# Kernel optimization log

Measured on AMD Instinct MI355X. Metric: run time of the kernel, lower is better.

## Reference

```python
import jax, jax.numpy as jnp
import numpy as np

B, L, D = 2, 4096, 1024
H = 8
DK = D // H          # 128 head qk dim (expand_k=1)
DV = 2 * D // H      # 256 head v dim (expand_v=2)
FFN = 4 * D          # 4096
CHUNK = 64
EPS = 1e-6


def _ln(x, w, b):
    mu = x.mean(-1, keepdims=True)
    var = ((x - mu) ** 2).mean(-1, keepdims=True)
    return (x - mu) / jnp.sqrt(var + EPS) * w + b


def _retention(q, k, v):
    # q,k: [B,H,L,DK], v: [B,H,L,DV]; RetNet decayed causal linear attention,
    # computed chunkwise (intra-chunk parallel + inter-chunk recurrent state).
    Bq, Hq, Lq, Dk = q.shape
    Dv = v.shape[-1]
    N = Lq // CHUNK
    b = 1.0 - jnp.exp2(-5.0 - jnp.arange(Hq, dtype=q.dtype))   # [H] per-head decay
    logb = jnp.log(b)
    q = q * (Dk ** -0.5)
    t = jnp.arange(CHUNK, dtype=q.dtype)
    diff = t[:, None] - t[None, :]                              # [C,C]
    mask = jnp.where(diff >= 0, jnp.exp(logb[:, None, None] * diff), 0.0)  # [H,C,C]
    d_q = jnp.exp(logb[:, None] * (t[None, :] + 1.0))           # b^(t+1), [H,C]
    d_k = jnp.exp(logb[:, None] * (CHUNK - 1.0 - t[None, :]))   # b^(C-1-s), [H,C]
    d_c = jnp.exp(logb * CHUNK)                                 # b^C, [H]

    def to_chunks(x):
        return x.reshape(Bq, Hq, N, CHUNK, -1).transpose(2, 0, 1, 3, 4)  # [N,B,H,C,d]

    qc, kc, vc = to_chunks(q), to_chunks(k), to_chunks(v)
    S0 = jnp.zeros((Bq, Hq, Dk, Dv), q.dtype)

    def step(S, inp):
        qi, ki, vi = inp                                        # [B,H,C,*]
        A = jnp.einsum('bhtd,bhsd->bhts', qi, ki) * mask        # intra-chunk scores
        o = jnp.einsum('bhts,bhsv->bhtv', A, vi)
        o = o + jnp.einsum('bhtd,bhdv->bhtv', qi * d_q[None, :, :, None], S)
        S = S * d_c[None, :, None, None] + jnp.einsum('bhsd,bhsv->bhdv', ki * d_k[None, :, :, None], vi)
        return S, o

    _, os = jax.lax.scan(step, S0, (qc, kc, vc))                # os: [N,B,H,C,DV]
    return os.transpose(1, 2, 0, 3, 4).reshape(Bq, Hq, Lq, Dv)


def setup_inputs() -> dict:
    key = jax.random.key(0)
    ks = jax.random.split(key, 8)
    s = 0.02
    return {
        'x': jax.random.normal(ks[0], (B, L, D), jnp.float32),
        'ln1_w': jnp.ones((D,), jnp.float32),
        'ln1_b': jnp.zeros((D,), jnp.float32),
        'Wq': jax.random.normal(ks[1], (D, D), jnp.float32) * s,
        'Wk': jax.random.normal(ks[2], (D, D), jnp.float32) * s,
        'Wv': jax.random.normal(ks[3], (D, 2 * D), jnp.float32) * s,
        'Wo': jax.random.normal(ks[4], (2 * D, D), jnp.float32) * s,
        'ln2_w': jnp.ones((D,), jnp.float32),
        'ln2_b': jnp.zeros((D,), jnp.float32),
        'W1': jax.random.normal(ks[5], (D, FFN), jnp.float32) * s,
        'b1': jnp.zeros((FFN,), jnp.float32),
        'W2': jax.random.normal(ks[6], (FFN, D), jnp.float32) * s,
        'b2': jnp.zeros((D,), jnp.float32),
    }


def reference(x, ln1_w, ln1_b, Wq, Wk, Wv, Wo, ln2_w, ln2_b, W1, b1, W2, b2):
    # retention branch
    h = _ln(x, ln1_w, ln1_b)
    q = (h @ Wq).reshape(B, L, H, DK).transpose(0, 2, 1, 3)
    k = (h @ Wk).reshape(B, L, H, DK).transpose(0, 2, 1, 3)
    v = (h @ Wv).reshape(B, L, H, DV).transpose(0, 2, 1, 3)
    o = _retention(q, k, v)                                      # [B,H,L,DV]
    o = o.transpose(0, 2, 1, 3).reshape(B, L, H * DV)
    x = x + o @ Wo
    # FFN branch (exact gelu, no subln, eval-mode dropout)
    f = _ln(x, ln2_w, ln2_b)
    f = jax.nn.gelu(f @ W1 + b1, approximate=False)
    x = x + (f @ W2 + b2)
    return x
```

## Files before the change

kernel.cpp:

```cpp
#include <hip/hip_runtime.h>
#include <math.h>

typedef short s16;
typedef __attribute__((ext_vector_type(8))) short short8;
typedef __attribute__((ext_vector_type(4))) float f32x4;

__device__ __forceinline__ float bf2f_lo(unsigned u){ return __builtin_bit_cast(float, u << 16); }
__device__ __forceinline__ float bf2f_hi(unsigned u){ return __builtin_bit_cast(float, u & 0xffff0000u); }
__device__ __forceinline__ float bf2f(unsigned short h){ return __builtin_bit_cast(float, (unsigned)h << 16); }
__device__ __forceinline__ s16 f2bf(float f){
  unsigned u = __builtin_bit_cast(unsigned, f);
  u += 0x7fffu + ((u >> 16) & 1u);
  return (s16)(u >> 16);
}
__device__ __forceinline__ void unpack8(int4 v, float* f){
  unsigned a=(unsigned)v.x, b=(unsigned)v.y, c=(unsigned)v.z, d=(unsigned)v.w;
  f[0]=bf2f_lo(a); f[1]=bf2f_hi(a); f[2]=bf2f_lo(b); f[3]=bf2f_hi(b);
  f[4]=bf2f_lo(c); f[5]=bf2f_hi(c); f[6]=bf2f_lo(d); f[7]=bf2f_hi(d);
}
__device__ __forceinline__ void gl2lds16(const s16* g, s16* l){
  __builtin_amdgcn_global_load_lds((const __attribute__((address_space(1))) void*)g,
                                   (__attribute__((address_space(3))) void*)l, 16, 0, 0);
}

__global__ __launch_bounds__(256) void ln_bf16(const float* __restrict__ x,
                                               const float* __restrict__ w,
                                               const float* __restrict__ b,
                                               s16* __restrict__ out){
  int row = blockIdx.x; int t = threadIdx.x;
  const float* xr = x + (size_t)row * 1024;
  float4 v = *(const float4*)(xr + t*4);
  float s = v.x + v.y + v.z + v.w;
  float ss = v.x*v.x + v.y*v.y + v.z*v.z + v.w*v.w;
  for (int o = 32; o > 0; o >>= 1){ s += __shfl_down(s, o, 64); ss += __shfl_down(ss, o, 64); }
  __shared__ float red[8];
  int wid = t >> 6, lane = t & 63;
  if (lane == 0){ red[wid] = s; red[4+wid] = ss; }
  __syncthreads();
  if (t == 0){
    float S = red[0]+red[1]+red[2]+red[3];
    float SS = red[4]+red[5]+red[6]+red[7];
    red[0] = S * (1.f/1024.f);
    red[1] = SS * (1.f/1024.f);
  }
  __syncthreads();
  float mu = red[0];
  float var = red[1] - mu*mu;
  float rstd = rsqrtf(var + 1e-6f);
  float vv[4] = {v.x, v.y, v.z, v.w};
  short4 o4;
  s16 tmp[4];
  #pragma unroll
  for (int i = 0; i < 4; ++i){
    int c = t*4 + i;
    float val = (vv[i] - mu) * rstd * w[c] + b[c];
    tmp[i] = f2bf(val);
  }
  o4.x = tmp[0]; o4.y = tmp[1]; o4.z = tmp[2]; o4.w = tmp[3];
  *(short4*)(out + (size_t)row*1024 + t*4) = o4;
}

__global__ __launch_bounds__(256) void conv_t(const float* __restrict__ W,
                                              s16* __restrict__ Wt,
                                              int K, int N, float scale){
  __shared__ float tile[32][33];
  int n0 = blockIdx.x * 32, k0 = blockIdx.y * 32;
  int tx = threadIdx.x & 31, ty = threadIdx.x >> 5;
  #pragma unroll
  for (int i = 0; i < 4; ++i){
    int r = ty + i*8;
    tile[r][tx] = W[(size_t)(k0 + r)*N + n0 + tx];
  }
  __syncthreads();
  #pragma unroll
  for (int i = 0; i < 4; ++i){
    int r = ty + i*8;
    Wt[(size_t)(n0 + r)*K + k0 + tx] = f2bf(tile[tx][r] * scale);
  }
}

__device__ __forceinline__ void xcd_tile(int tiles_y, int& tx, int& ty){
  int id = blockIdx.x;
  int sy = tiles_y >> 3;
  int xcd = id & 7, p = id >> 3;
  ty = xcd * sy + (p % sy);
  tx = p / sy;
}

__global__ __launch_bounds__(256,2) void gemm_nt(const s16* __restrict__ A,
                                                 const s16* __restrict__ Bt,
                                                 int M, int N, int K, int ldb,
                                                 float* __restrict__ Cf,
                                                 s16* __restrict__ Cb,
                                                 const float* __restrict__ bias,
                                                 const float* __restrict__ resid,
                                                 int flags, int tiles_y){
  __shared__ s16 As0[128*32], As1[128*32];
  __shared__ s16 Bs0[128*32], Bs1[128*32];
  int t = threadIdx.x;
  int tx, ty; xcd_tile(tiles_y, tx, ty);
  int m0 = ty * 128, n0 = tx * 128;
  int w = t >> 6, lane = t & 63;
  int wm = (w >> 1) * 64, wn = (w & 1) * 64;
  int lrow = lane & 15, lq = lane >> 4;
  f32x4 acc[4][4];
  #pragma unroll
  for (int i = 0; i < 4; ++i)
    #pragma unroll
    for (int j = 0; j < 4; ++j) acc[i][j] = (f32x4){0.f,0.f,0.f,0.f};

  const s16* Ag = A  + (size_t)(m0 + (t>>2)) * K   + (t&3)*8;
  const s16* Bg = Bt + (size_t)(n0 + (t>>2)) * ldb + (t&3)*8;
  int wo = w*512;

  for (int k0 = 0; k0 < K; k0 += 64){
    __syncthreads();
    gl2lds16(Ag + k0,                     As0 + wo);
    gl2lds16(Ag + (size_t)64*K + k0,      As0 + 2048 + wo);
    gl2lds16(Ag + k0 + 32,                As1 + wo);
    gl2lds16(Ag + (size_t)64*K + k0 + 32, As1 + 2048 + wo);
    gl2lds16(Bg + k0,                       Bs0 + wo);
    gl2lds16(Bg + (size_t)64*ldb + k0,      Bs0 + 2048 + wo);
    gl2lds16(Bg + k0 + 32,                  Bs1 + wo);
    gl2lds16(Bg + (size_t)64*ldb + k0 + 32, Bs1 + 2048 + wo);
    __syncthreads();
    short8 af[4], bfr[4];
    #pragma unroll
    for (int mi = 0; mi < 4; ++mi)
      af[mi] = *(short8*)&As0[(wm + mi*16 + lrow)*32 + lq*8];
    #pragma unroll
    for (int ni = 0; ni < 4; ++ni)
      bfr[ni] = *(short8*)&Bs0[(wn + ni*16 + lrow)*32 + lq*8];
    #pragma unroll
    for (int mi = 0; mi < 4; ++mi)
      #pragma unroll
      for (int ni = 0; ni < 4; ++ni)
        acc[mi][ni] = __builtin_amdgcn_mfma_f32_16x16x32_bf16(af[mi], bfr[ni], acc[mi][ni], 0, 0, 0);
    #pragma unroll
    for (int mi = 0; mi < 4; ++mi)
      af[mi] = *(short8*)&As1[(wm + mi*16 + lrow)*32 + lq*8];
    #pragma unroll
    for (int ni = 0; ni < 4; ++ni)
      bfr[ni] = *(short8*)&Bs1[(wn + ni*16 + lrow)*32 + lq*8];
    #pragma unroll
    for (int mi = 0; mi < 4; ++mi)
      #pragma unroll
      for (int ni = 0; ni < 4; ++ni)
        acc[mi][ni] = __builtin_amdgcn_mfma_f32_16x16x32_bf16(af[mi], bfr[ni], acc[mi][ni], 0, 0, 0);
  }

  bool do_gelu = flags & 1;
  bool out_bf = flags & 2;
  #pragma unroll
  for (int mi = 0; mi < 4; ++mi){
    #pragma unroll
    for (int ni = 0; ni < 4; ++ni){
      int gcol = n0 + wn + ni*16 + lrow;
      float bcol = bias ? bias[gcol] : 0.f;
      int grow_base = m0 + wm + mi*16 + lq*4;
      #pragma unroll
      for (int r = 0; r < 4; ++r){
        int grow = grow_base + r;
        float val = acc[mi][ni][r] + bcol;
        if (do_gelu) val = 0.5f * val * (1.f + erff(val * 0.70710678118654752f));
        if (resid) val += resid[(size_t)grow * N + gcol];
        if (out_bf) Cb[(size_t)grow * N + gcol] = f2bf(val);
        else        Cf[(size_t)grow * N + gcol] = val;
      }
    }
  }
}

__global__ __launch_bounds__(256,2) void gemm_nt_h(const s16* __restrict__ A,
                                                   const s16* __restrict__ Bt,
                                                   int M, int N, int K, int ldb,
                                                   float* __restrict__ Cf,
                                                   s16* __restrict__ Cb,
                                                   const float* __restrict__ bias,
                                                   const float* __restrict__ resid,
                                                   int flags, int tiles_y){
  __shared__ s16 As0[64*32], As1[64*32];
  __shared__ s16 Bs0[128*32], Bs1[128*32];
  int t = threadIdx.x;
  int tx, ty; xcd_tile(tiles_y, tx, ty);
  int m0 = ty * 64, n0 = tx * 128;
  int w = t >> 6, lane = t & 63;
  int lrow = lane & 15, lq = lane >> 4;
  f32x4 acc[4][2];
  #pragma unroll
  for (int i = 0; i < 4; ++i)
    #pragma unroll
    for (int j = 0; j < 2; ++j) acc[i][j] = (f32x4){0.f,0.f,0.f,0.f};

  const s16* Ag = A  + (size_t)(m0 + (t>>2)) * K   + (t&3)*8;
  const s16* Bg = Bt + (size_t)(n0 + (t>>2)) * ldb + (t&3)*8;
  int wo = w*512;

  for (int k0 = 0; k0 < K; k0 += 64){
    __syncthreads();
    gl2lds16(Ag + k0,      As0 + wo);
    gl2lds16(Ag + k0 + 32, As1 + wo);
    gl2lds16(Bg + k0,                       Bs0 + wo);
    gl2lds16(Bg + (size_t)64*ldb + k0,      Bs0 + 2048 + wo);
    gl2lds16(Bg + k0 + 32,                  Bs1 + wo);
    gl2lds16(Bg + (size_t)64*ldb + k0 + 32, Bs1 + 2048 + wo);
    __syncthreads();
    short8 af[4], bfr[2];
    #pragma unroll
    for (int mi = 0; mi < 4; ++mi)
      af[mi] = *(short8*)&As0[(mi*16 + lrow)*32 + lq*8];
    #pragma unroll
    for (int ni = 0; ni < 2; ++ni)
      bfr[ni] = *(short8*)&Bs0[(w*32 + ni*16 + lrow)*32 + lq*8];
    #pragma unroll
    for (int mi = 0; mi < 4; ++mi)
      #pragma unroll
      for (int ni = 0; ni < 2; ++ni)
        acc[mi][ni] = __builtin_amdgcn_mfma_f32_16x16x32_bf16(af[mi], bfr[ni], acc[mi][ni], 0, 0, 0);
    #pragma unroll
    for (int mi = 0; mi < 4; ++mi)
      af[mi] = *(short8*)&As1[(mi*16 + lrow)*32 + lq*8];
    #pragma unroll
    for (int ni = 0; ni < 2; ++ni)
      bfr[ni] = *(short8*)&Bs1[(w*32 + ni*16 + lrow)*32 + lq*8];
    #pragma unroll
    for (int mi = 0; mi < 4; ++mi)
      #pragma unroll
      for (int ni = 0; ni < 2; ++ni)
        acc[mi][ni] = __builtin_amdgcn_mfma_f32_16x16x32_bf16(af[mi], bfr[ni], acc[mi][ni], 0, 0, 0);
  }

  bool do_gelu = flags & 1;
  bool out_bf = flags & 2;
  #pragma unroll
  for (int mi = 0; mi < 4; ++mi){
    #pragma unroll
    for (int ni = 0; ni < 2; ++ni){
      int gcol = n0 + w*32 + ni*16 + lrow;
      float bcol = bias ? bias[gcol] : 0.f;
      int grow_base = m0 + mi*16 + lq*4;
      #pragma unroll
      for (int r = 0; r < 4; ++r){
        int grow = grow_base + r;
        float val = acc[mi][ni][r] + bcol;
        if (do_gelu) val = 0.5f * val * (1.f + erff(val * 0.70710678118654752f));
        if (resid) val += resid[(size_t)grow * N + gcol];
        if (out_bf) Cb[(size_t)grow * N + gcol] = f2bf(val);
        else        Cf[(size_t)grow * N + gcol] = val;
      }
    }
  }
}

__global__ __launch_bounds__(256,2) void ret_chunksum(const s16* __restrict__ k,
                                                      const s16* __restrict__ v,
                                                      s16* __restrict__ U){
  int bi = blockIdx.x;
  int h = bi & 7, n = bi >> 3;
  int t = threadIdx.x;
  __shared__ s16 ks[128*72];
  __shared__ s16 vs[256*72];
  float log2b = log2f(1.f - exp2f(-5.f - (float)h));
  const s16* kbase = k + (size_t)(n*64)*4096 + h*128;
  const s16* vbase = v + (size_t)(n*64)*4096 + h*256;
  #pragma unroll
  for (int i = 0; i < 4; ++i){
    int e = i*2048 + t*8;
    int s = e >> 7, dk = e & 127;
    int4 kv = *(const int4*)(kbase + (size_t)s*4096 + dk);
    float f[8]; unpack8(kv, f);
    float dec = exp2f(log2b * (float)(63 - s));
    #pragma unroll
    for (int j = 0; j < 8; ++j) ks[(dk+j)*72 + s] = f2bf(f[j]*dec);
  }
  #pragma unroll
  for (int i = 0; i < 8; ++i){
    int e = i*2048 + t*8;
    int s = e >> 8, dv = e & 255;
    int4 vv = *(const int4*)(vbase + (size_t)s*4096 + dv);
    s16 tmp[8]; *(int4*)tmp = vv;
    #pragma unroll
    for (int j = 0; j < 8; ++j) vs[(dv+j)*72 + s] = tmp[j];
  }
  __syncthreads();
  int w = t >> 6, lane = t & 63;
  int m0w = w*64;
  int lrow = lane & 15, lq = lane >> 4;
  f32x4 acc[4][8];
  #pragma unroll
  for (int mi = 0; mi < 4; ++mi)
    #pragma unroll
    for (int ni = 0; ni < 8; ++ni) acc[mi][ni] = (f32x4){0.f,0.f,0.f,0.f};
  #pragma unroll
  for (int kk = 0; kk < 64; kk += 32){
    short8 af[4], bfr[8];
    #pragma unroll
    for (int mi = 0; mi < 4; ++mi)
      af[mi] = *(short8*)&vs[(m0w + mi*16 + lrow)*72 + kk + lq*8];
    #pragma unroll
    for (int ni = 0; ni < 8; ++ni)
      bfr[ni] = *(short8*)&ks[(ni*16 + lrow)*72 + kk + lq*8];
    #pragma unroll
    for (int mi = 0; mi < 4; ++mi)
      #pragma unroll
      for (int ni = 0; ni < 8; ++ni)
        acc[mi][ni] = __builtin_amdgcn_mfma_f32_16x16x32_bf16(af[mi], bfr[ni], acc[mi][ni], 0, 0, 0);
  }
  s16* Ub = U + ((size_t)(h*64 + n))*32768;
  #pragma unroll
  for (int mi = 0; mi < 4; ++mi)
    #pragma unroll
    for (int ni = 0; ni < 8; ++ni)
      #pragma unroll
      for (int r = 0; r < 4; ++r){
        int row = m0w + mi*16 + lq*4 + r;
        int col = ni*16 + lrow;
        Ub[(size_t)row*128 + col] = f2bf(acc[mi][ni][r]);
      }
}

__global__ __launch_bounds__(256) void ret_scan(s16* __restrict__ US){
  int tid = blockIdx.x*256 + threadIdx.x;
  int h = tid >> 12;
  int rem = tid & 4095;
  int dv = rem >> 4, dk0 = (rem & 15)*8;
  float log2b = log2f(1.f - exp2f(-5.f - (float)h));
  float dc = exp2f(log2b * 64.f);
  s16* base = US + (size_t)h*64*32768 + (size_t)dv*128 + dk0;
  float acc[8] = {0.f,0.f,0.f,0.f,0.f,0.f,0.f,0.f};
  #pragma unroll 4
  for (int n = 0; n < 64; ++n){
    s16* p = base + (size_t)n*32768;
    int4 u4 = *(const int4*)p;
    float uf[8]; unpack8(u4, uf);
    s16 sb[8];
    #pragma unroll
    for (int j = 0; j < 8; ++j) sb[j] = f2bf(acc[j]);
    *(int4*)p = *(int4*)sb;
    #pragma unroll
    for (int j = 0; j < 8; ++j) acc[j] = acc[j]*dc + uf[j];
  }
}

__global__ __launch_bounds__(256,2) void ret_attn(const s16* __restrict__ q,
                                                  const s16* __restrict__ k,
                                                  const s16* __restrict__ v,
                                                  const s16* __restrict__ S,
                                                  s16* __restrict__ o){
  int bi = blockIdx.x;
  int h = bi & 7, n = bi >> 3;
  int t = threadIdx.x;
  int w = t >> 6, lane = t & 63;
  int lrow = lane & 15, lq = lane >> 4;
  float log2b = log2f(1.f - exp2f(-5.f - (float)h));
  __shared__ s16 As[64*72];
  __shared__ s16 vs[256*72];

  const s16* vbase = v + (size_t)(n*64)*4096 + h*256;
  #pragma unroll
  for (int i = 0; i < 8; ++i){
    int e = i*2048 + t*8;
    int s = e >> 8, dv = e & 255;
    int4 vv = *(const int4*)(vbase + (size_t)s*4096 + dv);
    s16 tmp[8]; *(int4*)tmp = vv;
    #pragma unroll
    for (int j = 0; j < 8; ++j) vs[(dv+j)*72 + s] = tmp[j];
  }

  const s16* qbase = q + (size_t)(n*64)*4096 + h*128;
  const s16* kbase = k + (size_t)(n*64)*4096 + h*128;
  short8 qf[4][4];
  #pragma unroll
  for (int ti = 0; ti < 4; ++ti)
    #pragma unroll
    for (int c = 0; c < 4; ++c)
      qf[ti][c] = *(const short8*)(qbase + (size_t)(ti*16 + lrow)*4096 + c*32 + lq*8);
  short8 kf[4];
  #pragma unroll
  for (int c = 0; c < 4; ++c)
    kf[c] = *(const short8*)(kbase + (size_t)(16*w + lrow)*4096 + c*32 + lq*8);
  #pragma unroll
  for (int ti = 0; ti < 4; ++ti){
    f32x4 acc_a = (f32x4){0.f,0.f,0.f,0.f};
    #pragma unroll
    for (int c = 0; c < 4; ++c)
      acc_a = __builtin_amdgcn_mfma_f32_16x16x32_bf16(qf[ti][c], kf[c], acc_a, 0, 0, 0);
    #pragma unroll
    for (int r = 0; r < 4; ++r){
      int ti_idx = ti*16 + lq*4 + r;
      int s_idx = 16*w + lrow;
      int d = ti_idx - s_idx;
      float val = (d >= 0) ? acc_a[r] * exp2f(log2b * (float)d) : 0.f;
      As[ti_idx*72 + s_idx] = f2bf(val);
    }
  }
  __syncthreads();

  f32x4 acc[4][4];
  #pragma unroll
  for (int mi = 0; mi < 4; ++mi)
    #pragma unroll
    for (int nj = 0; nj < 4; ++nj) acc[mi][nj] = (f32x4){0.f,0.f,0.f,0.f};

  const s16* Sbase = S + ((size_t)(h*64 + n)*256 + w*64)*128;
  #pragma unroll
  for (int c = 0; c < 4; ++c){
    short8 bf[4];
    #pragma unroll
    for (int nj = 0; nj < 4; ++nj)
      bf[nj] = *(const short8*)(Sbase + (size_t)(nj*16 + lrow)*128 + c*32 + lq*8);
    #pragma unroll
    for (int mi = 0; mi < 4; ++mi)
      #pragma unroll
      for (int nj = 0; nj < 4; ++nj)
        acc[mi][nj] = __builtin_amdgcn_mfma_f32_16x16x32_bf16(qf[mi][c], bf[nj], acc[mi][nj], 0, 0, 0);
  }
  #pragma unroll
  for (int mi = 0; mi < 4; ++mi){
    #pragma unroll
    for (int r = 0; r < 4; ++r){
      float dq = exp2f(log2b * (float)(mi*16 + lq*4 + r + 1));
      #pragma unroll
      for (int nj = 0; nj < 4; ++nj) acc[mi][nj][r] *= dq;
    }
  }
  #pragma unroll
  for (int c = 0; c < 2; ++c){
    short8 af[4], bf[4];
    #pragma unroll
    for (int mi = 0; mi < 4; ++mi)
      af[mi] = *(short8*)&As[(mi*16 + lrow)*72 + c*32 + lq*8];
    #pragma unroll
    for (int nj = 0; nj < 4; ++nj)
      bf[nj] = *(short8*)&vs[(w*64 + nj*16 + lrow)*72 + c*32 + lq*8];
    #pragma unroll
    for (int mi = 0; mi < 4; ++mi)
      #pragma unroll
      for (int nj = 0; nj < 4; ++nj)
        acc[mi][nj] = __builtin_amdgcn_mfma_f32_16x16x32_bf16(af[mi], bf[nj], acc[mi][nj], 0, 0, 0);
  }
  s16* obase = o + (size_t)(n*64)*2048 + h*256;
  #pragma unroll
  for (int mi = 0; mi < 4; ++mi)
    #pragma unroll
    for (int nj = 0; nj < 4; ++nj)
      #pragma unroll
      for (int r = 0; r < 4; ++r){
        int row = mi*16 + lq*4 + r;
        int col = w*64 + nj*16 + lrow;
        obase[(size_t)row*2048 + col] = f2bf(acc[mi][nj][r]);
      }
}

extern "C" void kernel_launch(void* const* d_in, const int* in_sizes, int n_in,
                              void* d_out, int out_size, void* d_ws, size_t ws_size,
                              hipStream_t stream) {
  (void)in_sizes; (void)n_in; (void)out_size; (void)ws_size;
  const float* x     = (const float*)d_in[0];
  const float* ln1_w = (const float*)d_in[1];
  const float* ln1_b = (const float*)d_in[2];
  const float* Wq    = (const float*)d_in[3];
  const float* Wk    = (const float*)d_in[4];
  const float* Wv    = (const float*)d_in[5];
  const float* Wo    = (const float*)d_in[6];
  const float* ln2_w = (const float*)d_in[7];
  const float* ln2_b = (const float*)d_in[8];
  const float* W1    = (const float*)d_in[9];
  const float* b1    = (const float*)d_in[10];
  const float* W2    = (const float*)d_in[11];
  const float* b2    = (const float*)d_in[12];
  float* out = (float*)d_out;
  char* ws = (char*)d_ws;

  const size_t MB = 1ull << 20;
  s16* Wqkv_t = (s16*)(ws + 0*MB);
  s16* Wo_t = (s16*)(ws + 8*MB);
  s16* W1_t = (s16*)(ws + 12*MB);
  s16* W2_t = (s16*)(ws + 20*MB);
  s16* hbuf = (s16*)(ws + 28*MB);
  s16* h2   = (s16*)(ws + 28*MB);
  s16* qkv  = (s16*)(ws + 44*MB);
  float* x1 = (float*)(ws + 44*MB);
  s16* fb   = (s16*)(ws + 76*MB);
  s16* US   = (s16*)(ws + 108*MB);
  s16* ob   = (s16*)(ws + 140*MB);

  conv_t<<<dim3(32,32),  256, 0, stream>>>(Wq, Wqkv_t, 1024, 1024, 0.08838834764831845f);
  conv_t<<<dim3(32,32),  256, 0, stream>>>(Wk, Wqkv_t + (size_t)1024*1024, 1024, 1024, 1.f);
  conv_t<<<dim3(64,32),  256, 0, stream>>>(Wv, Wqkv_t + (size_t)2048*1024, 1024, 2048, 1.f);
  conv_t<<<dim3(32,64),  256, 0, stream>>>(Wo, Wo_t, 2048, 1024, 1.f);
  conv_t<<<dim3(128,32), 256, 0, stream>>>(W1, W1_t, 1024, 4096, 1.f);
  conv_t<<<dim3(32,128), 256, 0, stream>>>(W2, W2_t, 4096, 1024, 1.f);

  ln_bf16<<<8192, 256, 0, stream>>>(x, ln1_w, ln1_b, hbuf);

  gemm_nt<<<2048, 256, 0, stream>>>(hbuf, Wqkv_t, 8192, 4096, 1024, 1024, nullptr, qkv, nullptr, nullptr, 2, 64);

  for (int b = 0; b < 2; ++b){
    const s16* q_b = qkv + (size_t)b*4096*4096;
    const s16* k_b = q_b + 1024;
    const s16* v_b = q_b + 2048;
    s16* ob_b = ob + (size_t)b*4096*2048;
    ret_chunksum<<<512, 256, 0, stream>>>(k_b, v_b, US);
    ret_scan<<<128, 256, 0, stream>>>(US);
    ret_attn<<<512, 256, 0, stream>>>(q_b, k_b, v_b, US, ob_b);
  }

  gemm_nt_h<<<1024, 256, 0, stream>>>(ob, Wo_t, 8192, 1024, 2048, 2048, x1, nullptr, nullptr, x, 0, 128);
  ln_bf16<<<8192, 256, 0, stream>>>(x1, ln2_w, ln2_b, h2);

  gemm_nt<<<2048, 256, 0, stream>>>(h2, W1_t, 8192, 4096, 1024, 1024, nullptr, fb, b1, nullptr, 2|1, 64);
  gemm_nt_h<<<1024, 256, 0, stream>>>(fb, W2_t, 8192, 1024, 4096, 4096, out, nullptr, b2, x1, 0, 128);
}
```

Baseline: 612.7 us.

## Replace 128x128 GEMM with 256x256 double-buffered swizzled-LDS GEMM for QKV and FFN1

The two bf16-output GEMMs (QKV projection and FFN up-projection with GELU) move from a 128x128 tile, 256-thread kernel to a 256x256 tile, 512-thread kernel. The new kernel double-buffers LDS with asynchronous global-to-LDS loads, splits each K step into four quadrant MFMA phases interleaved with the next tile's loads, and uses an XOR-swizzled LDS layout and s_setprio. The aim is more data reuse per tile, fewer LDS bank conflicts, and overlap of memory loads with MFMA work. In exchange it uses 128KB of LDS and one block per CU, and relies on hand-written vmcnt and barrier bookkeeping that must stay correct.

```diff
diff --git a/kernel.cpp b/kernel.cpp
--- a/kernel.cpp
+++ b/kernel.cpp
@@ -87,85 +87,131 @@
   tx = p / sy;
 }
 
-__global__ __launch_bounds__(256,2) void gemm_nt(const s16* __restrict__ A,
+__global__ __launch_bounds__(512,2) void gemm256(const s16* __restrict__ A,
                                                  const s16* __restrict__ Bt,
-                                                 int M, int N, int K, int ldb,
-                                                 float* __restrict__ Cf,
+                                                 int N, int K,
                                                  s16* __restrict__ Cb,
                                                  const float* __restrict__ bias,
-                                                 const float* __restrict__ resid,
                                                  int flags, int tiles_y){
-  __shared__ s16 As0[128*32], As1[128*32];
-  __shared__ s16 Bs0[128*32], Bs1[128*32];
+  __shared__ s16 lds[2*4*8192];
   int t = threadIdx.x;
   int tx, ty; xcd_tile(tiles_y, tx, ty);
-  int m0 = ty * 128, n0 = tx * 128;
+  int m0 = ty * 256, n0 = tx * 256;
   int w = t >> 6, lane = t & 63;
-  int wm = (w >> 1) * 64, wn = (w & 1) * 64;
+  int wm = w >> 2, wn = w & 3;
   int lrow = lane & 15, lq = lane >> 4;
-  f32x4 acc[4][4];
-  #pragma unroll
-  for (int i = 0; i < 4; ++i)
-    #pragma unroll
-    for (int j = 0; j < 4; ++j) acc[i][j] = (f32x4){0.f,0.f,0.f,0.f};
-
-  const s16* Ag = A  + (size_t)(m0 + (t>>2)) * K   + (t&3)*8;
-  const s16* Bg = Bt + (size_t)(n0 + (t>>2)) * ldb + (t&3)*8;
-  int wo = w*512;
-
-  for (int k0 = 0; k0 < K; k0 += 64){
-    __syncthreads();
-    gl2lds16(Ag + k0,                     As0 + wo);
-    gl2lds16(Ag + (size_t)64*K + k0,      As0 + 2048 + wo);
-    gl2lds16(Ag + k0 + 32,                As1 + wo);
-    gl2lds16(Ag + (size_t)64*K + k0 + 32, As1 + 2048 + wo);
-    gl2lds16(Bg + k0,                       Bs0 + wo);
-    gl2lds16(Bg + (size_t)64*ldb + k0,      Bs0 + 2048 + wo);
-    gl2lds16(Bg + k0 + 32,                  Bs1 + wo);
-    gl2lds16(Bg + (size_t)64*ldb + k0 + 32, Bs1 + 2048 + wo);
-    __syncthreads();
-    short8 af[4], bfr[4];
-    #pragma unroll
-    for (int mi = 0; mi < 4; ++mi)
-      af[mi] = *(short8*)&As0[(wm + mi*16 + lrow)*32 + lq*8];
-    #pragma unroll
-    for (int ni = 0; ni < 4; ++ni)
-      bfr[ni] = *(short8*)&Bs0[(wn + ni*16 + lrow)*32 + lq*8];
-    #pragma unroll
-    for (int mi = 0; mi < 4; ++mi)
-      #pragma unroll
-      for (int ni = 0; ni < 4; ++ni)
-        acc[mi][ni] = __builtin_amdgcn_mfma_f32_16x16x32_bf16(af[mi], bfr[ni], acc[mi][ni], 0, 0, 0);
-    #pragma unroll
-    for (int mi = 0; mi < 4; ++mi)
-      af[mi] = *(short8*)&As1[(wm + mi*16 + lrow)*32 + lq*8];
-    #pragma unroll
-    for (int ni = 0; ni < 4; ++ni)
-      bfr[ni] = *(short8*)&Bs1[(wn + ni*16 + lrow)*32 + lq*8];
-    #pragma unroll
-    for (int mi = 0; mi < 4; ++mi)
-      #pragma unroll
-      for (int ni = 0; ni < 4; ++ni)
-        acc[mi][ni] = __builtin_amdgcn_mfma_f32_16x16x32_bf16(af[mi], bfr[ni], acc[mi][ni], 0, 0, 0);
-  }
+  int s = lrow & 7;
+
+  int grow = t >> 3;
+  int g = (t & 7) ^ (grow & 7);
+  const s16* Ag = A  + (size_t)(m0 + grow) * K + g*8;
+  const s16* Bg = Bt + (size_t)(n0 + grow) * K + g*8;
+  int wo = w * 512;
+
+  int abase = (wm*64 + lrow) * 64;
+  int bbase = (wn*32 + lrow) * 64;
+  int sw0 = ((lq ^ s) << 3);
+  int sw1 = (((4 + lq) ^ s) << 3);
+
+  f32x4 acc[2][4][2][2];
+  #pragma unroll
+  for (int a = 0; a < 2; ++a)
+    #pragma unroll
+    for (int b = 0; b < 4; ++b)
+      #pragma unroll
+      for (int c = 0; c < 2; ++c)
+        #pragma unroll
+        for (int d = 0; d < 2; ++d) acc[a][b][c][d] = (f32x4){0.f,0.f,0.f,0.f};
+
+  short8 af[2][4];
+  short8 bfr[2][2][2];
+
+#define STG_A(buf,h,kt) do{ \
+    gl2lds16(Ag + (size_t)((h)*128    )*K + (kt)*64, lds + ((buf)*4+(h))*8192 + wo); \
+    gl2lds16(Ag + (size_t)((h)*128+ 64)*K + (kt)*64, lds + ((buf)*4+(h))*8192 + 4096 + wo); }while(0)
+#define STG_B(buf,nh,kt) do{ \
+    gl2lds16(Bg + (size_t)((nh)*128    )*K + (kt)*64, lds + ((buf)*4+2+(nh))*8192 + wo); \
+    gl2lds16(Bg + (size_t)((nh)*128+ 64)*K + (kt)*64, lds + ((buf)*4+2+(nh))*8192 + 4096 + wo); }while(0)
+#define RD_A(buf,mh) do{ const s16* p_ = lds + ((buf)*4+(mh))*8192 + abase; \
+    _Pragma("unroll") for (int m_ = 0; m_ < 4; ++m_){ \
+      af[0][m_] = *(const short8*)(p_ + m_*1024 + sw0); \
+      af[1][m_] = *(const short8*)(p_ + m_*1024 + sw1); } }while(0)
+#define RD_B(buf,nh) do{ const s16* p_ = lds + ((buf)*4+2+(nh))*8192 + bbase; \
+    _Pragma("unroll") for (int n_ = 0; n_ < 2; ++n_){ \
+      bfr[nh][0][n_] = *(const short8*)(p_ + n_*1024 + sw0); \
+      bfr[nh][1][n_] = *(const short8*)(p_ + n_*1024 + sw1); } }while(0)
+#define MFMA_Q(mh,nh) do{ __builtin_amdgcn_s_setprio(1); \
+    _Pragma("unroll") for (int kk_ = 0; kk_ < 2; ++kk_) \
+      _Pragma("unroll") for (int m_ = 0; m_ < 4; ++m_) \
+        _Pragma("unroll") for (int n_ = 0; n_ < 2; ++n_) \
+          acc[mh][m_][nh][n_] = __builtin_amdgcn_mfma_f32_16x16x32_bf16( \
+              af[kk_][m_], bfr[nh][kk_][n_], acc[mh][m_][nh][n_], 0, 0, 0); \
+    __builtin_amdgcn_s_setprio(0); }while(0)
+#define VM6() asm volatile("s_waitcnt vmcnt(6)" ::: "memory")
+#define BARR() asm volatile("s_barrier" ::: "memory")
+
+  int NT = K >> 6;
+  STG_A(0,0,0); STG_B(0,0,0); STG_B(0,1,0); STG_A(0,1,0);
+
+  for (int kt = 0; kt < NT-1; ++kt){
+    int cb = kt & 1, nb = cb ^ 1;
+    STG_A(nb,0,kt+1);
+    VM6(); BARR();
+    RD_A(cb,0); RD_B(cb,0);
+    MFMA_Q(0,0);
+    BARR();
+    STG_B(nb,0,kt+1);
+    VM6(); BARR();
+    RD_B(cb,1);
+    MFMA_Q(0,1);
+    BARR();
+    STG_B(nb,1,kt+1);
+    VM6(); BARR();
+    RD_A(cb,1);
+    MFMA_Q(1,0);
+    BARR();
+    STG_A(nb,1,kt+1);
+    BARR();
+    MFMA_Q(1,1);
+    BARR();
+  }
+  {
+    int cb = (NT-1) & 1;
+    asm volatile("s_waitcnt vmcnt(4)" ::: "memory"); BARR();
+    RD_A(cb,0); RD_B(cb,0); MFMA_Q(0,0); BARR();
+    asm volatile("s_waitcnt vmcnt(2)" ::: "memory"); BARR();
+    RD_B(cb,1); MFMA_Q(0,1); BARR();
+    asm volatile("s_waitcnt vmcnt(0)" ::: "memory"); BARR();
+    RD_A(cb,1); MFMA_Q(1,0); BARR();
+    MFMA_Q(1,1);
+  }
+#undef STG_A
+#undef STG_B
+#undef RD_A
+#undef RD_B
+#undef MFMA_Q
+#undef VM6
+#undef BARR
 
   bool do_gelu = flags & 1;
-  bool out_bf = flags & 2;
-  #pragma unroll
-  for (int mi = 0; mi < 4; ++mi){
-    #pragma unroll
-    for (int ni = 0; ni < 4; ++ni){
-      int gcol = n0 + wn + ni*16 + lrow;
-      float bcol = bias ? bias[gcol] : 0.f;
-      int grow_base = m0 + wm + mi*16 + lq*4;
-      #pragma unroll
-      for (int r = 0; r < 4; ++r){
-        int grow = grow_base + r;
-        float val = acc[mi][ni][r] + bcol;
-        if (do_gelu) val = 0.5f * val * (1.f + erff(val * 0.70710678118654752f));
-        if (resid) val += resid[(size_t)grow * N + gcol];
-        if (out_bf) Cb[(size_t)grow * N + gcol] = f2bf(val);
-        else        Cf[(size_t)grow * N + gcol] = val;
+  #pragma unroll
+  for (int nh = 0; nh < 2; ++nh){
+    #pragma unroll
+    for (int nj = 0; nj < 2; ++nj){
+      int col = n0 + wn*32 + nh*128 + nj*16 + lrow;
+      float bcol = bias ? bias[col] : 0.f;
+      #pragma unroll
+      for (int mh = 0; mh < 2; ++mh){
+        #pragma unroll
+        for (int m = 0; m < 4; ++m){
+          int row_base = m0 + wm*64 + mh*128 + m*16 + lq*4;
+          #pragma unroll
+          for (int r = 0; r < 4; ++r){
+            float val = acc[mh][m][nh][nj][r] + bcol;
+            if (do_gelu) val = 0.5f * val * (1.f + erff(val * 0.70710678118654752f));
+            Cb[(size_t)(row_base + r) * N + col] = f2bf(val);
+          }
+        }
       }
     }
   }
@@ -494,7 +540,7 @@
 
   ln_bf16<<<8192, 256, 0, stream>>>(x, ln1_w, ln1_b, hbuf);
 
-  gemm_nt<<<2048, 256, 0, stream>>>(hbuf, Wqkv_t, 8192, 4096, 1024, 1024, nullptr, qkv, nullptr, nullptr, 2, 64);
+  gemm256<<<512, 512, 0, stream>>>(hbuf, Wqkv_t, 4096, 1024, qkv, nullptr, 0, 32);
 
   for (int b = 0; b < 2; ++b){
     const s16* q_b = qkv + (size_t)b*4096*4096;
@@ -509,6 +555,6 @@
   gemm_nt_h<<<1024, 256, 0, stream>>>(ob, Wo_t, 8192, 1024, 2048, 2048, x1, nullptr, nullptr, x, 0, 128);
   ln_bf16<<<8192, 256, 0, stream>>>(x1, ln2_w, ln2_b, h2);
 
-  gemm_nt<<<2048, 256, 0, stream>>>(h2, W1_t, 8192, 4096, 1024, 1024, nullptr, fb, b1, nullptr, 2|1, 64);
+  gemm256<<<512, 512, 0, stream>>>(h2, W1_t, 4096, 1024, fb, b1, 1, 32);
   gemm_nt_h<<<1024, 256, 0, stream>>>(fb, W2_t, 8192, 1024, 4096, 4096, out, nullptr, b2, x1, 0, 128);
 }
```

Result: no change. 623.1 us (+1.7%).
